# Kernel tuning notes

Hardware: AMD Instinct MI355X
Metric: run time of the kernel (lower is better)

## Reference

```python
import jax, jax.numpy as jnp
import numpy as np

ALPHA = 0.2   # LeakyReLU negative slope
NEG = -9e15   # mask fill value from the torch code


def _conv1d(x, w, b):
    # x: (N, C_in, L), w: (C_out, C_in, 5), padding=2 -> same length
    y = jax.lax.conv_general_dilated(x, w, window_strides=(1,), padding=[(2, 2)],
                                     dimension_numbers=('NCH', 'OIH', 'NCH'))
    return y + b[None, :, None]


def _gat(h, mask, W, a):
    # Faithful to a_input @ a: e_ij = leakyrelu(Wh_i . a[:H] + Wh_j . a[H:])
    Wh = jnp.einsum('bnf,fo->bno', h, W)          # (B,N,H)
    H = W.shape[1]
    f1 = Wh @ a[:H]                               # (B,N,1)
    f2 = Wh @ a[H:]                               # (B,N,1)
    e = f1 + jnp.swapaxes(f2, 1, 2)               # (B,N,N)
    e = jnp.where(e > 0, e, ALPHA * e)            # LeakyReLU
    e = jnp.where(mask, e, NEG)
    att = jax.nn.softmax(e, axis=-1)              # dropout skipped (eval mode)
    return jnp.einsum('bij,bjo->bio', att, Wh)


def setup_inputs() -> dict:
    key = jax.random.key(0)
    ks = jax.random.split(key, 14)
    B, S, N, H, E = 8, 200, 512, 64, 2048
    sc = 0.1
    return {
        'x': jax.random.normal(ks[0], (B, S, N * 2), dtype=jnp.float32),
        'adj': jax.random.randint(ks[1], (N, N), 0, 2, dtype=jnp.int32),
        'edge_index': jax.random.randint(ks[2], (E, 2), 0, N, dtype=jnp.int32),
        'conv1_w': jax.random.normal(ks[3], (H // 2, 2, 5), dtype=jnp.float32) * sc,
        'conv1_b': jnp.zeros((H // 2,), dtype=jnp.float32),
        'conv2_w': jax.random.normal(ks[4], (H, H // 2, 5), dtype=jnp.float32) * sc,
        'conv2_b': jnp.zeros((H,), dtype=jnp.float32),
        'W1': jax.random.normal(ks[5], (H, H), dtype=jnp.float32) * sc,
        'a1': jax.random.normal(ks[6], (2 * H, 1), dtype=jnp.float32) * sc,
        'W2': jax.random.normal(ks[7], (H, H), dtype=jnp.float32) * sc,
        'a2': jax.random.normal(ks[8], (2 * H, 1), dtype=jnp.float32) * sc,
        'fc1_w': jax.random.normal(ks[9], (2 * H, H), dtype=jnp.float32) * sc,
        'fc1_b': jnp.zeros((H,), dtype=jnp.float32),
        'fc2_w': jax.random.normal(ks[10], (H, 1), dtype=jnp.float32) * sc,
        'fc2_b': jnp.zeros((1,), dtype=jnp.float32),
    }


def reference(x, adj, edge_index, conv1_w, conv1_b, conv2_w, conv2_b,
              W1, a1, W2, a2, fc1_w, fc1_b, fc2_w, fc2_b):
    B = x.shape[0]
    N = adj.shape[0]
    # (B,S,2N) -> (B,N,S,2) -> (B*N,2,S)
    xn = x.reshape(B, -1, N, 2).transpose(0, 2, 1, 3)
    xf = xn.reshape(B * N, -1, 2).transpose(0, 2, 1)
    h = jax.nn.relu(_conv1d(xf, conv1_w, conv1_b))
    h = jax.nn.relu(_conv1d(h, conv2_w, conv2_b))
    h = h.mean(axis=-1)                 # AdaptiveAvgPool1d(1) + squeeze
    h = h.reshape(B, N, -1)             # (B,N,H)
    mask = (adj > 0)[None]              # (1,N,N) broadcasts over batch
    h = jax.nn.relu(_gat(h, mask, W1, a1))
    h = _gat(h, mask, W2, a2)
    h1 = h[:, edge_index[:, 0]]         # (B,E,H)
    h2 = h[:, edge_index[:, 1]]
    he = jnp.concatenate([h1, h2], axis=-1)  # (B,E,2H)
    z = jax.nn.relu(he @ fc1_w + fc1_b)
    return jax.nn.sigmoid(z @ fc2_w + fc2_b).squeeze(-1)  # (B,E)
```

## Files before the change

kernel.cpp:

```cpp
#include <hip/hip_runtime.h>
#include <hip/hip_bf16.h>

typedef unsigned short u16;
typedef __attribute__((ext_vector_type(8))) short short8;
typedef __attribute__((ext_vector_type(4))) float float4v;

#define BATCH 8
#define SLEN  200
#define NNODE 512
#define NEDGE 2048
#define NEGV  -9000000000000000.0f

#define H1S 40
#define H1R 212

__device__ __forceinline__ u16 f2bf(float f) {
    unsigned int x = __float_as_uint(f);
    unsigned int lsb = (x >> 16) & 1u;
    x += 0x7fffu + lsb;
    return (u16)(x >> 16);
}

__device__ __forceinline__ float bf2f(u16 u) {
    return __uint_as_float(((unsigned int)u) << 16);
}

__device__ __forceinline__ unsigned int pk2(float a, float b) {
    __hip_bfloat162 h = __float22bfloat162_rn(make_float2(a, b));
    unsigned int r;
    __builtin_memcpy(&r, &h, 4);
    return r;
}

__global__ __launch_bounds__(256) void pre_kernel(
    const float* __restrict__ x,
    const int* __restrict__ adj,
    const float* __restrict__ w2,
    const float* __restrict__ fc1w,
    const float* __restrict__ W2g,
    float* __restrict__ xT,
    u16* __restrict__ w2f,
    u16* __restrict__ efw,
    u16* __restrict__ w2gf,
    u16* __restrict__ msk)
{
    __shared__ float tile[32][33];
    const int t = threadIdx.x;
    const int blk = blockIdx.x;

    if (blk < 1792) {
        const int xi  = blk & 31;
        const int rem = blk >> 5;
        const int yi  = rem % 7;
        const int zi  = rem / 7;
        const int nc0 = xi * 32;
        const int s0  = yi * 32;
        const int c   = t & 31, rr = t >> 5;
        #pragma unroll
        for (int r = 0; r < 4; ++r) {
            const int s = s0 + rr + r * 8;
            if (s < SLEN)
                tile[rr + r * 8][c] = x[((size_t)(zi * SLEN + s)) * 1024 + nc0 + c];
        }
        __syncthreads();
        #pragma unroll
        for (int r = 0; r < 4; ++r) {
            const int nc = nc0 + rr + r * 8;
            const int s = s0 + c;
            if (s < SLEN)
                xT[((size_t)(zi * 1024 + nc)) * SLEN + s] = tile[c][rr + r * 8];
        }
        return;
    }

    if (blk == 1792) {
        for (int idx = t; idx < 20 * 64 * 8; idx += 256) {
            const int fid = idx >> 9, rem = idx & 511;
            const int lane = rem >> 3, j = rem & 7;
            const int kk = fid >> 2, ot = fid & 3;
            const int ml = lane & 15, q = lane >> 4;
            const int c  = q * 8 + j;
            const int ic = (c & 1) * 16 + (c >> 1);
            const int oc = ot * 16 + ml;
            w2f[idx] = f2bf(w2[(size_t)oc * 160 + ic * 5 + kk]);
        }
        return;
    }
    if (blk == 1793) {
        for (int idx = t; idx < 16 * 64 * 8; idx += 256) {
            const int u = idx >> 9, rem = idx & 511;
            const int lane = rem >> 3, j = rem & 7;
            const int ks = u >> 2, wvv = u & 3;
            const int ml = lane & 15, q = lane >> 4;
            const int o = wvv * 16 + ml;
            const int k = ks * 32 + q * 8 + j;
            efw[idx] = f2bf(fc1w[k * 64 + o]);
        }
        return;
    }
    if (blk == 1794) {
        for (int idx = t; idx < 8 * 64 * 8; idx += 256) {
            const int u = idx >> 9, rem = idx & 511;
            const int lane = rem >> 3, j = rem & 7;
            const int kh = u >> 2, nt = u & 3;
            const int ml = lane & 15, q = lane >> 4;
            const int o = nt * 16 + ml;
            const int k = kh * 32 + q * 8 + j;
            w2gf[idx] = f2bf(W2g[k * 64 + o]);
        }
        return;
    }

    {
        const int tid   = (blk - 1795) * 256 + t;
        const int row   = tid >> 5;
        const int chunk = tid & 31;
        const int4* ap = (const int4*)(adj + (size_t)row * 512 + chunk * 16);
        const int4 a0 = ap[0], a1 = ap[1], a2 = ap[2], a3 = ap[3];
        unsigned int bits = 0;
        bits |= (a0.x > 0) ? 0x0001u : 0u;  bits |= (a0.y > 0) ? 0x0002u : 0u;
        bits |= (a0.z > 0) ? 0x0004u : 0u;  bits |= (a0.w > 0) ? 0x0008u : 0u;
        bits |= (a1.x > 0) ? 0x0010u : 0u;  bits |= (a1.y > 0) ? 0x0020u : 0u;
        bits |= (a1.z > 0) ? 0x0040u : 0u;  bits |= (a1.w > 0) ? 0x0080u : 0u;
        bits |= (a2.x > 0) ? 0x0100u : 0u;  bits |= (a2.y > 0) ? 0x0200u : 0u;
        bits |= (a2.z > 0) ? 0x0400u : 0u;  bits |= (a2.w > 0) ? 0x0800u : 0u;
        bits |= (a3.x > 0) ? 0x1000u : 0u;  bits |= (a3.y > 0) ? 0x2000u : 0u;
        bits |= (a3.z > 0) ? 0x4000u : 0u;  bits |= (a3.w > 0) ? 0x8000u : 0u;
        msk[row * 32 + chunk] = (u16)bits;
    }
}

__global__ __launch_bounds__(256) void conv_fused_kernel(
    const float* __restrict__ xT,
    const float* __restrict__ w1,
    const float* __restrict__ b1,
    const float* __restrict__ b2,
    const float* __restrict__ W1,
    const float* __restrict__ a1,
    const u16* __restrict__ w2f,
    u16* __restrict__ Wh_bt,
    float* __restrict__ f1,
    float* __restrict__ f2)
{
    __shared__ float xs[2][2][212];
    __shared__ __align__(16) u16 h1p[H1R * H1S];
    __shared__ float red[4][2][32];
    __shared__ float hm[2][64];
    __shared__ float part[2][4][64];

    const int t    = threadIdx.x;
    const int blk  = blockIdx.x;
    const int b    = blk >> 8;
    const int pair = blk & 255;
    const int n0   = pair * 2;
    const int lane = t & 63;
    const int wv   = t >> 6;
    const int ml   = lane & 15;
    const int q    = lane >> 4;
    const int p = t & 15;
    const int g = t >> 4;
    const int o2 = wv & 1;
    const int mh = wv >> 1;

    short8 wfA[5], wfB[5];
    #pragma unroll
    for (int kk = 0; kk < 5; ++kk) {
        wfA[kk] = *(const short8*)(w2f + ((kk * 4 + o2 * 2 + 0) * 64 + lane) * 8);
        wfB[kk] = *(const short8*)(w2f + ((kk * 4 + o2 * 2 + 1) * 64 + lane) * 8);
    }
    const float bias2a = b2[o2 * 32 + ml];
    const float bias2b = b2[o2 * 32 + 16 + ml];

    float wA[10], wB[10];
    #pragma unroll
    for (int j = 0; j < 10; ++j) {
        wA[j] = w1[p * 10 + j];
        wB[j] = w1[(16 + p) * 10 + j];
    }
    const float b1a = b1[p], b1b = b1[16 + p];

    if (t < SLEN) {
        const float* xp = xT + ((size_t)(b * 1024 + 4 * pair)) * SLEN + t;
        xs[0][0][2 + t] = xp[0];
        xs[0][1][2 + t] = xp[SLEN];
        xs[1][0][2 + t] = xp[2 * SLEN];
        xs[1][1][2 + t] = xp[3 * SLEN];
    } else if (t < 212) {
        const int pp = (t < 202) ? (t - 200) : t;
        xs[0][0][pp] = 0.f; xs[0][1][pp] = 0.f;
        xs[1][0][pp] = 0.f; xs[1][1][pp] = 0.f;
    }
    {
        unsigned int* hz = (unsigned int*)h1p;
        if (t < 40)       hz[t] = 0u;
        else if (t < 240) hz[4000 + t] = 0u;
    }
    __syncthreads();

    float tAn[2], tBn[2];
    for (int nd = 0; nd < 2; ++nd) {
        #pragma unroll
        for (int u = 0; u < 4; ++u) {
            const int base = 4 * g + 64 * u;
            if (base < SLEN) {
                float X0[8], X1[8];
                *(float4*)&X0[0] = *(const float4*)&xs[nd][0][base];
                *(float4*)&X0[4] = *(const float4*)&xs[nd][0][base + 4];
                *(float4*)&X1[0] = *(const float4*)&xs[nd][1][base];
                *(float4*)&X1[4] = *(const float4*)&xs[nd][1][base + 4];
                #pragma unroll
                for (int i = 0; i < 4; ++i) {
                    float a0 = b1a, a1v = b1b;
                    #pragma unroll
                    for (int k = 0; k < 5; ++k) {
                        const float x0 = X0[i + k], x1 = X1[i + k];
                        a0  += wA[k] * x0 + wA[5 + k] * x1;
                        a1v += wB[k] * x0 + wB[5 + k] * x1;
                    }
                    *(unsigned int*)&h1p[(2 + base + i) * H1S + 2 * p] =
                        pk2(fmaxf(a0, 0.f), fmaxf(a1v, 0.f));
                }
            }
        }
        __syncthreads();

        float tA = 0.f, tB = 0.f;
        const int mt0 = mh * 7, mtE = mh ? 13 : 7;
        for (int mt = mt0; mt < mtE; ++mt) {
            float4v acc0 = {0.f, 0.f, 0.f, 0.f};
            float4v acc1 = {0.f, 0.f, 0.f, 0.f};
            #pragma unroll
            for (int kk = 0; kk < 5; ++kk) {
                const short8 a = *(const short8*)&h1p[(mt * 16 + ml + kk) * H1S + q * 8];
                acc0 = __builtin_amdgcn_mfma_f32_16x16x32_bf16(a, wfA[kk], acc0, 0, 0, 0);
                acc1 = __builtin_amdgcn_mfma_f32_16x16x32_bf16(a, wfB[kk], acc1, 0, 0, 0);
            }
            if (mt < 12) {
                #pragma unroll
                for (int r = 0; r < 4; ++r) {
                    tA += fmaxf(acc0[r] + bias2a, 0.f);
                    tB += fmaxf(acc1[r] + bias2b, 0.f);
                }
            } else if (q < 2) {
                #pragma unroll
                for (int r = 0; r < 4; ++r) {
                    tA += fmaxf(acc0[r] + bias2a, 0.f);
                    tB += fmaxf(acc1[r] + bias2b, 0.f);
                }
            }
        }
        tA += __shfl_xor(tA, 16, 64);
        tA += __shfl_xor(tA, 32, 64);
        tB += __shfl_xor(tB, 16, 64);
        tB += __shfl_xor(tB, 32, 64);
        tAn[nd] = tA;
        tBn[nd] = tB;
        __syncthreads();
    }

    if (lane < 16) {
        red[wv][0][ml]      = tAn[0];
        red[wv][0][16 + ml] = tBn[0];
        red[wv][1][ml]      = tAn[1];
        red[wv][1][16 + ml] = tBn[1];
    }
    __syncthreads();
    if (t < 128) {
        const int nd = t >> 6, o = t & 63;
        const int grp = (o >> 5), idx = o & 31;
        hm[nd][o] = (red[grp][nd][idx] + red[grp + 2][nd][idx]) * (1.0f / 200.0f);
    }
    __syncthreads();

    {
        const int o = t & 63, q4 = t >> 6;
        const float* Wp = W1 + (q4 * 16) * 64 + o;
        float p0 = 0.f, p1 = 0.f;
        #pragma unroll
        for (int k = 0; k < 16; ++k) {
            const float w = Wp[k * 64];
            p0 += hm[0][q4 * 16 + k] * w;
            p1 += hm[1][q4 * 16 + k] * w;
        }
        part[0][q4][o] = p0;
        part[1][q4][o] = p1;
    }
    __syncthreads();
    if (t < 128) {
        const int nd = t >> 6, o = t & 63;
        const int n = n0 + nd;
        const float v = part[nd][0][o] + part[nd][1][o] + part[nd][2][o] + part[nd][3][o];
        Wh_bt[((size_t)(b * 64 + o)) * 512 + n] = f2bf(v);
        float v1 = v * a1[o];
        float v2 = v * a1[64 + o];
        #pragma unroll
        for (int off = 32; off; off >>= 1) {
            v1 += __shfl_xor(v1, off, 64);
            v2 += __shfl_xor(v2, off, 64);
        }
        if (o == 0) { f1[b * 512 + n] = v1; f2[b * 512 + n] = v2; }
    }
}

#define PSTR 520
__global__ __launch_bounds__(512) void gat_attn_kernel(
    const u16* __restrict__ Wh_bt,
    const float* __restrict__ f1in,
    const float* __restrict__ f2in,
    const u16* __restrict__ msk,
    const u16* __restrict__ w2gf,
    const float* __restrict__ a2,
    u16* __restrict__ whbt_out,
    float* __restrict__ f1out,
    float* __restrict__ f2out,
    float* __restrict__ outp,
    const int fuse)
{
    __shared__ __align__(16) u16 P[16 * PSTR];
    __shared__ float f2s[512];
    __shared__ float invs[16];
    __shared__ float f1s[16];
    __shared__ float accH[4][64][4];
    __shared__ __align__(16) u16 g1s[16 * 72];
    __shared__ __align__(16) u16 wh2s[64 * 20];
    __shared__ float fp1[4][16], fp2[4][16];

    const int t   = threadIdx.x;
    const int blk = blockIdx.x;
    const int b   = blk >> 5;
    const int i0  = (blk & 31) * 16;
    const int lane = t & 63, wv = t >> 6, nt = wv & 3, kh = wv >> 2;
    const int ml = lane & 15, q = lane >> 4;

    const u16* Bp = Wh_bt + ((size_t)(b * 64 + nt * 16 + ml)) * 512 + kh * 256 + q * 8;
    short8 bfr[8];
    #pragma unroll
    for (int ks = 0; ks < 8; ++ks)
        bfr[ks] = *(const short8*)(Bp + ks * 32);

    f2s[t & 511] = f2in[b * 512 + (t & 511)];
    if (t < 16) f1s[t] = f1in[b * 512 + i0 + t];
    __syncthreads();

    {
        const int i = t >> 5, jseg = t & 31;
        const float f1i = f1s[i];
        const unsigned int mbits = msk[(size_t)(i0 + i) * 32 + jseg];
        const float* f2p = f2s + jseg * 16;
        float ev[16];
        float mx = -3.0e38f;
        #pragma unroll
        for (int v = 0; v < 16; ++v) {
            float e = f1i + f2p[v];
            e = e > 0.f ? e : 0.2f * e;
            e = ((mbits >> v) & 1u) ? e : NEGV;
            ev[v] = e;
            mx = fmaxf(mx, e);
        }
        mx = fmaxf(mx, __shfl_xor(mx, 1, 64));
        mx = fmaxf(mx, __shfl_xor(mx, 2, 64));
        mx = fmaxf(mx, __shfl_xor(mx, 4, 64));
        mx = fmaxf(mx, __shfl_xor(mx, 8, 64));
        mx = fmaxf(mx, __shfl_xor(mx, 16, 64));
        float sum = 0.f;
        #pragma unroll
        for (int v = 0; v < 16; ++v) {
            const float ex = __expf(ev[v] - mx);
            ev[v] = ex;
            sum += ex;
        }
        sum += __shfl_xor(sum, 1, 64);
        sum += __shfl_xor(sum, 2, 64);
        sum += __shfl_xor(sum, 4, 64);
        sum += __shfl_xor(sum, 8, 64);
        sum += __shfl_xor(sum, 16, 64);
        if (jseg == 0) invs[i] = 1.0f / sum;
        unsigned int* prow = (unsigned int*)&P[i * PSTR + jseg * 16];
        #pragma unroll
        for (int v = 0; v < 8; ++v)
            prow[v] = pk2(ev[2 * v], ev[2 * v + 1]);
    }
    __syncthreads();

    float4v acc = {0.f, 0.f, 0.f, 0.f};
    #pragma unroll
    for (int ks = 0; ks < 8; ++ks) {
        const short8 afr = *(const short8*)&P[ml * PSTR + kh * 256 + ks * 32 + q * 8];
        acc = __builtin_amdgcn_mfma_f32_16x16x32_bf16(afr, bfr[ks], acc, 0, 0, 0);
    }
    if (kh == 1) {
        #pragma unroll
        for (int r = 0; r < 4; ++r) accH[nt][lane][r] = acc[r];
    }
    __syncthreads();
    if (kh == 0) {
        #pragma unroll
        for (int r = 0; r < 4; ++r) {
            const int i2 = q * 4 + r;
            float val = (acc[r] + accH[nt][lane][r]) * invs[i2];
            if (fuse) {
                val = fmaxf(val, 0.f);
                g1s[i2 * 72 + nt * 16 + ml] = f2bf(val);
            } else {
                outp[((size_t)(b * 512 + i0 + i2)) * 64 + nt * 16 + ml] = val;
            }
        }
    }

    if (!fuse) return;

    __syncthreads();
    const short8 af2 = *(const short8*)&g1s[ml * 72 + kh * 32 + q * 8];
    const short8 bf2v = *(const short8*)(w2gf + ((kh * 4 + nt) * 64 + lane) * 8);
    float4v c2 = {0.f, 0.f, 0.f, 0.f};
    c2 = __builtin_amdgcn_mfma_f32_16x16x32_bf16(af2, bf2v, c2, 0, 0, 0);
    if (kh == 1) {
        #pragma unroll
        for (int r = 0; r < 4; ++r) accH[nt][lane][r] = c2[r];
    }
    __syncthreads();
    if (kh == 0) {
        const int o = nt * 16 + ml;
        const float a2o1 = a2[o], a2o2 = a2[64 + o];
        #pragma unroll
        for (int r = 0; r < 4; ++r) {
            const float wv2 = c2[r] + accH[nt][lane][r];
            wh2s[o * 20 + q * 4 + r] = f2bf(wv2);
            float p1 = wv2 * a2o1, p2 = wv2 * a2o2;
            p1 += __shfl_xor(p1, 1, 64); p2 += __shfl_xor(p2, 1, 64);
            p1 += __shfl_xor(p1, 2, 64); p2 += __shfl_xor(p2, 2, 64);
            p1 += __shfl_xor(p1, 4, 64); p2 += __shfl_xor(p2, 4, 64);
            p1 += __shfl_xor(p1, 8, 64); p2 += __shfl_xor(p2, 8, 64);
            if (ml == 0) {
                fp1[nt][q * 4 + r] = p1;
                fp2[nt][q * 4 + r] = p2;
            }
        }
    }
    __syncthreads();
    if (t < 256) {
        const int o = t >> 2, seg = t & 3;
        *(uint2*)&whbt_out[((size_t)(b * 64 + o)) * 512 + i0 + seg * 4] =
            *(const uint2*)&wh2s[o * 20 + seg * 4];
    }
    if (t < 16) {
        f1out[b * 512 + i0 + t] = fp1[0][t] + fp1[1][t] + fp1[2][t] + fp1[3][t];
        f2out[b * 512 + i0 + t] = fp2[0][t] + fp2[1][t] + fp2[2][t] + fp2[3][t];
    }
}

#define FSTR 136
__global__ __launch_bounds__(256) void edge_mlp_kernel(
    const float* __restrict__ hg,
    const int* __restrict__ eidx,
    const u16* __restrict__ efw,
    const float* __restrict__ fc1b,
    const float* __restrict__ fc2w,
    const float* __restrict__ fc2b,
    float* __restrict__ out)
{
    __shared__ __align__(16) u16 he[16 * FSTR];
    __shared__ float part[16][4];

    const int t   = threadIdx.x;
    const int blk = blockIdx.x;
    const int b   = blk >> 7;
    const int e0  = (blk & 127) * 16;
    const int lane = t & 63, wv = t >> 6, ml = lane & 15, q = lane >> 4;

    short8 bw[4];
    #pragma unroll
    for (int ks = 0; ks < 4; ++ks)
        bw[ks] = *(const short8*)(efw + ((ks * 4 + wv) * 64 + lane) * 8);
    const int o = 16 * wv + ml;
    const float bo = fc1b[o];
    const float wo = fc2w[o];

    {
        const int ep = t >> 4, p = t & 15;
        const int e = e0 + ep;
        const int node = (p < 8) ? eidx[e * 2] : eidx[e * 2 + 1];
        const int c0 = (p & 7) * 8;
        const float* hp = hg + ((size_t)(b * 512 + node)) * 64 + c0;
        const float4 fa = *(const float4*)hp;
        const float4 fb = *(const float4*)(hp + 4);
        unsigned int* dst = (unsigned int*)&he[ep * FSTR + ((p < 8) ? 0 : 64) + c0];
        dst[0] = pk2(fa.x, fa.y);
        dst[1] = pk2(fa.z, fa.w);
        dst[2] = pk2(fb.x, fb.y);
        dst[3] = pk2(fb.z, fb.w);
    }
    __syncthreads();

    float4v acc = {0.f, 0.f, 0.f, 0.f};
    #pragma unroll
    for (int ks = 0; ks < 4; ++ks) {
        const short8 afr = *(const short8*)&he[ml * FSTR + ks * 32 + q * 8];
        acc = __builtin_amdgcn_mfma_f32_16x16x32_bf16(afr, bw[ks], acc, 0, 0, 0);
    }
    #pragma unroll
    for (int r = 0; r < 4; ++r) {
        float z = fmaxf(acc[r] + bo, 0.f) * wo;
        z += __shfl_xor(z, 1, 64);
        z += __shfl_xor(z, 2, 64);
        z += __shfl_xor(z, 4, 64);
        z += __shfl_xor(z, 8, 64);
        if (ml == 0) part[q * 4 + r][wv] = z;
    }
    __syncthreads();
    if (t < 16) {
        const float v = part[t][0] + part[t][1] + part[t][2] + part[t][3] + fc2b[0];
        out[b * 2048 + e0 + t] = 1.0f / (1.0f + __expf(-v));
    }
}

extern "C" void kernel_launch(void* const* d_in, const int* in_sizes, int n_in,
                              void* d_out, int out_size, void* d_ws, size_t ws_size,
                              hipStream_t stream) {
    const float* x    = (const float*)d_in[0];
    const int* adj    = (const int*)d_in[1];
    const int* eidx   = (const int*)d_in[2];
    const float* w1   = (const float*)d_in[3];
    const float* b1   = (const float*)d_in[4];
    const float* w2   = (const float*)d_in[5];
    const float* b2   = (const float*)d_in[6];
    const float* W1   = (const float*)d_in[7];
    const float* a1   = (const float*)d_in[8];
    const float* W2   = (const float*)d_in[9];
    const float* a2   = (const float*)d_in[10];
    const float* fc1w = (const float*)d_in[11];
    const float* fc1b = (const float*)d_in[12];
    const float* fc2w = (const float*)d_in[13];
    const float* fc2b = (const float*)d_in[14];
    float* out = (float*)d_out;

    float* ws = (float*)d_ws;
    const size_t R = (size_t)BATCH * NNODE;
    float* g     = ws;
    float* f1a   = g + R * 64;
    float* f2a   = f1a + R;
    float* f1b   = f2a + R;
    float* f2b   = f1b + R;
    u16*   whbt1 = (u16*)(f2b + R);
    u16*   whbt2 = whbt1 + R * 64;
    u16*   w2f   = whbt2 + R * 64;
    u16*   efw   = w2f + 10240;
    u16*   w2gf  = efw + 8192;
    u16*   msk   = w2gf + 4096;
    float* xT    = (float*)(msk + 16384);

    pre_kernel<<<dim3(1859), dim3(256), 0, stream>>>(
        x, adj, w2, fc1w, W2, xT, w2f, efw, w2gf, msk);
    conv_fused_kernel<<<dim3(2048), dim3(256), 0, stream>>>(
        xT, w1, b1, b2, W1, a1, w2f, whbt1, f1a, f2a);
    gat_attn_kernel<<<dim3(256), dim3(512), 0, stream>>>(
        whbt1, f1a, f2a, msk, w2gf, a2, whbt2, f1b, f2b, g, 1);
    gat_attn_kernel<<<dim3(256), dim3(512), 0, stream>>>(
        whbt2, f1b, f2b, msk, w2gf, a2, whbt2, f1b, f2b, g, 0);
    edge_mlp_kernel<<<dim3(1024), dim3(256), 0, stream>>>(
        g, eidx, efw, fc1b, fc2w, fc2b, out);
}
```

Before: 136.6 us.

## Drop x transpose pass and fuse both GAT layers with edge MLP cooperatively

The separate transpose of x into xT is removed. The conv kernel now reads four contiguous floats per timestep directly from x with a float4 load. The two GAT attention launches and the edge MLP launch are merged into one cooperative kernel that uses grid-wide syncs between layers, and each block handles 64 edges in the MLP stage. This removes a full-size transpose write/read and two kernel launches. In exchange, x reads become strided in the conv kernel, and the merged kernel pays for grid syncs and a larger shared-memory footprint.

Result: slower. 279.8 us (+104.9%).

```diff
diff --git a/kernel.cpp b/kernel.cpp
--- a/kernel.cpp
+++ b/kernel.cpp
@@ -1,5 +1,8 @@
 #include <hip/hip_runtime.h>
 #include <hip/hip_bf16.h>
+#include <hip/hip_cooperative_groups.h>
+
+namespace cg = cooperative_groups;
 
 typedef unsigned short u16;
 typedef __attribute__((ext_vector_type(8))) short short8;
@@ -33,47 +36,19 @@
 }
 
 __global__ __launch_bounds__(256) void pre_kernel(
-    const float* __restrict__ x,
     const int* __restrict__ adj,
     const float* __restrict__ w2,
     const float* __restrict__ fc1w,
     const float* __restrict__ W2g,
-    float* __restrict__ xT,
     u16* __restrict__ w2f,
     u16* __restrict__ efw,
     u16* __restrict__ w2gf,
     u16* __restrict__ msk)
 {
-    __shared__ float tile[32][33];
     const int t = threadIdx.x;
     const int blk = blockIdx.x;
 
-    if (blk < 1792) {
-        const int xi  = blk & 31;
-        const int rem = blk >> 5;
-        const int yi  = rem % 7;
-        const int zi  = rem / 7;
-        const int nc0 = xi * 32;
-        const int s0  = yi * 32;
-        const int c   = t & 31, rr = t >> 5;
-        #pragma unroll
-        for (int r = 0; r < 4; ++r) {
-            const int s = s0 + rr + r * 8;
-            if (s < SLEN)
-                tile[rr + r * 8][c] = x[((size_t)(zi * SLEN + s)) * 1024 + nc0 + c];
-        }
-        __syncthreads();
-        #pragma unroll
-        for (int r = 0; r < 4; ++r) {
-            const int nc = nc0 + rr + r * 8;
-            const int s = s0 + c;
-            if (s < SLEN)
-                xT[((size_t)(zi * 1024 + nc)) * SLEN + s] = tile[c][rr + r * 8];
-        }
-        return;
-    }
-
-    if (blk == 1792) {
+    if (blk == 0) {
         for (int idx = t; idx < 20 * 64 * 8; idx += 256) {
             const int fid = idx >> 9, rem = idx & 511;
             const int lane = rem >> 3, j = rem & 7;
@@ -86,7 +61,7 @@
         }
         return;
     }
-    if (blk == 1793) {
+    if (blk == 1) {
         for (int idx = t; idx < 16 * 64 * 8; idx += 256) {
             const int u = idx >> 9, rem = idx & 511;
             const int lane = rem >> 3, j = rem & 7;
@@ -98,7 +73,7 @@
         }
         return;
     }
-    if (blk == 1794) {
+    if (blk == 2) {
         for (int idx = t; idx < 8 * 64 * 8; idx += 256) {
             const int u = idx >> 9, rem = idx & 511;
             const int lane = rem >> 3, j = rem & 7;
@@ -112,7 +87,7 @@
     }
 
     {
-        const int tid   = (blk - 1795) * 256 + t;
+        const int tid   = (blk - 3) * 256 + t;
         const int row   = tid >> 5;
         const int chunk = tid & 31;
         const int4* ap = (const int4*)(adj + (size_t)row * 512 + chunk * 16);
@@ -131,7 +106,7 @@
 }
 
 __global__ __launch_bounds__(256) void conv_fused_kernel(
-    const float* __restrict__ xT,
+    const float* __restrict__ x,
     const float* __restrict__ w1,
     const float* __restrict__ b1,
     const float* __restrict__ b2,
@@ -180,11 +155,11 @@
     const float b1a = b1[p], b1b = b1[16 + p];
 
     if (t < SLEN) {
-        const float* xp = xT + ((size_t)(b * 1024 + 4 * pair)) * SLEN + t;
-        xs[0][0][2 + t] = xp[0];
-        xs[0][1][2 + t] = xp[SLEN];
-        xs[1][0][2 + t] = xp[2 * SLEN];
-        xs[1][1][2 + t] = xp[3 * SLEN];
+        const float4 xv = *(const float4*)(x + ((size_t)(b * SLEN + t)) * 1024 + 4 * pair);
+        xs[0][0][2 + t] = xv.x;
+        xs[0][1][2 + t] = xv.y;
+        xs[1][0][2 + t] = xv.z;
+        xs[1][1][2 + t] = xv.w;
     } else if (t < 212) {
         const int pp = (t < 202) ? (t - 200) : t;
         xs[0][0][pp] = 0.f; xs[0][1][pp] = 0.f;
@@ -303,19 +278,27 @@
 }
 
 #define PSTR 520
-__global__ __launch_bounds__(512) void gat_attn_kernel(
-    const u16* __restrict__ Wh_bt,
-    const float* __restrict__ f1in,
-    const float* __restrict__ f2in,
+#define FSTR 136
+__global__ __launch_bounds__(512) void gat_edge_kernel(
+    const u16* __restrict__ Wh1,
+    const float* __restrict__ f1a,
+    const float* __restrict__ f2a,
     const u16* __restrict__ msk,
     const u16* __restrict__ w2gf,
     const float* __restrict__ a2,
-    u16* __restrict__ whbt_out,
-    float* __restrict__ f1out,
-    float* __restrict__ f2out,
-    float* __restrict__ outp,
-    const int fuse)
+    u16* __restrict__ Wh2,
+    float* __restrict__ f1b,
+    float* __restrict__ f2b,
+    float* __restrict__ g,
+    const int* __restrict__ eidx,
+    const u16* __restrict__ efw,
+    const float* __restrict__ fc1b,
+    const float* __restrict__ fc2w,
+    const float* __restrict__ fc2b,
+    float* __restrict__ out)
 {
+    cg::grid_group gg = cg::this_grid();
+
     __shared__ __align__(16) u16 P[16 * PSTR];
     __shared__ float f2s[512];
     __shared__ float invs[16];
@@ -324,6 +307,8 @@
     __shared__ __align__(16) u16 g1s[16 * 72];
     __shared__ __align__(16) u16 wh2s[64 * 20];
     __shared__ float fp1[4][16], fp2[4][16];
+    __shared__ __align__(16) u16 he[64 * FSTR];
+    __shared__ float epart[4][16][4];
 
     const int t   = threadIdx.x;
     const int blk = blockIdx.x;
@@ -332,159 +317,150 @@
     const int lane = t & 63, wv = t >> 6, nt = wv & 3, kh = wv >> 2;
     const int ml = lane & 15, q = lane >> 4;
 
-    const u16* Bp = Wh_bt + ((size_t)(b * 64 + nt * 16 + ml)) * 512 + kh * 256 + q * 8;
-    short8 bfr[8];
-    #pragma unroll
-    for (int ks = 0; ks < 8; ++ks)
-        bfr[ks] = *(const short8*)(Bp + ks * 32);
-
-    f2s[t & 511] = f2in[b * 512 + (t & 511)];
-    if (t < 16) f1s[t] = f1in[b * 512 + i0 + t];
-    __syncthreads();
-
-    {
-        const int i = t >> 5, jseg = t & 31;
-        const float f1i = f1s[i];
-        const unsigned int mbits = msk[(size_t)(i0 + i) * 32 + jseg];
-        const float* f2p = f2s + jseg * 16;
-        float ev[16];
-        float mx = -3.0e38f;
-        #pragma unroll
-        for (int v = 0; v < 16; ++v) {
-            float e = f1i + f2p[v];
-            e = e > 0.f ? e : 0.2f * e;
-            e = ((mbits >> v) & 1u) ? e : NEGV;
-            ev[v] = e;
-            mx = fmaxf(mx, e);
-        }
-        mx = fmaxf(mx, __shfl_xor(mx, 1, 64));
-        mx = fmaxf(mx, __shfl_xor(mx, 2, 64));
-        mx = fmaxf(mx, __shfl_xor(mx, 4, 64));
-        mx = fmaxf(mx, __shfl_xor(mx, 8, 64));
-        mx = fmaxf(mx, __shfl_xor(mx, 16, 64));
-        float sum = 0.f;
-        #pragma unroll
-        for (int v = 0; v < 16; ++v) {
-            const float ex = __expf(ev[v] - mx);
-            ev[v] = ex;
-            sum += ex;
-        }
-        sum += __shfl_xor(sum, 1, 64);
-        sum += __shfl_xor(sum, 2, 64);
-        sum += __shfl_xor(sum, 4, 64);
-        sum += __shfl_xor(sum, 8, 64);
-        sum += __shfl_xor(sum, 16, 64);
-        if (jseg == 0) invs[i] = 1.0f / sum;
-        unsigned int* prow = (unsigned int*)&P[i * PSTR + jseg * 16];
-        #pragma unroll
-        for (int v = 0; v < 8; ++v)
-            prow[v] = pk2(ev[2 * v], ev[2 * v + 1]);
-    }
-    __syncthreads();
-
-    float4v acc = {0.f, 0.f, 0.f, 0.f};
-    #pragma unroll
-    for (int ks = 0; ks < 8; ++ks) {
-        const short8 afr = *(const short8*)&P[ml * PSTR + kh * 256 + ks * 32 + q * 8];
-        acc = __builtin_amdgcn_mfma_f32_16x16x32_bf16(afr, bfr[ks], acc, 0, 0, 0);
-    }
-    if (kh == 1) {
-        #pragma unroll
-        for (int r = 0; r < 4; ++r) accH[nt][lane][r] = acc[r];
-    }
-    __syncthreads();
-    if (kh == 0) {
-        #pragma unroll
-        for (int r = 0; r < 4; ++r) {
-            const int i2 = q * 4 + r;
-            float val = (acc[r] + accH[nt][lane][r]) * invs[i2];
-            if (fuse) {
-                val = fmaxf(val, 0.f);
-                g1s[i2 * 72 + nt * 16 + ml] = f2bf(val);
-            } else {
-                outp[((size_t)(b * 512 + i0 + i2)) * 64 + nt * 16 + ml] = val;
-            }
-        }
-    }
-
-    if (!fuse) return;
-
-    __syncthreads();
-    const short8 af2 = *(const short8*)&g1s[ml * 72 + kh * 32 + q * 8];
-    const short8 bf2v = *(const short8*)(w2gf + ((kh * 4 + nt) * 64 + lane) * 8);
-    float4v c2 = {0.f, 0.f, 0.f, 0.f};
-    c2 = __builtin_amdgcn_mfma_f32_16x16x32_bf16(af2, bf2v, c2, 0, 0, 0);
-    if (kh == 1) {
-        #pragma unroll
-        for (int r = 0; r < 4; ++r) accH[nt][lane][r] = c2[r];
-    }
-    __syncthreads();
-    if (kh == 0) {
-        const int o = nt * 16 + ml;
-        const float a2o1 = a2[o], a2o2 = a2[64 + o];
-        #pragma unroll
-        for (int r = 0; r < 4; ++r) {
-            const float wv2 = c2[r] + accH[nt][lane][r];
-            wh2s[o * 20 + q * 4 + r] = f2bf(wv2);
-            float p1 = wv2 * a2o1, p2 = wv2 * a2o2;
-            p1 += __shfl_xor(p1, 1, 64); p2 += __shfl_xor(p2, 1, 64);
-            p1 += __shfl_xor(p1, 2, 64); p2 += __shfl_xor(p2, 2, 64);
-            p1 += __shfl_xor(p1, 4, 64); p2 += __shfl_xor(p2, 4, 64);
-            p1 += __shfl_xor(p1, 8, 64); p2 += __shfl_xor(p2, 8, 64);
-            if (ml == 0) {
-                fp1[nt][q * 4 + r] = p1;
-                fp2[nt][q * 4 + r] = p2;
-            }
-        }
-    }
-    __syncthreads();
-    if (t < 256) {
-        const int o = t >> 2, seg = t & 3;
-        *(uint2*)&whbt_out[((size_t)(b * 64 + o)) * 512 + i0 + seg * 4] =
-            *(const uint2*)&wh2s[o * 20 + seg * 4];
-    }
-    if (t < 16) {
-        f1out[b * 512 + i0 + t] = fp1[0][t] + fp1[1][t] + fp1[2][t] + fp1[3][t];
-        f2out[b * 512 + i0 + t] = fp2[0][t] + fp2[1][t] + fp2[2][t] + fp2[3][t];
-    }
-}
-
-#define FSTR 136
-__global__ __launch_bounds__(256) void edge_mlp_kernel(
-    const float* __restrict__ hg,
-    const int* __restrict__ eidx,
-    const u16* __restrict__ efw,
-    const float* __restrict__ fc1b,
-    const float* __restrict__ fc2w,
-    const float* __restrict__ fc2b,
-    float* __restrict__ out)
-{
-    __shared__ __align__(16) u16 he[16 * FSTR];
-    __shared__ float part[16][4];
-
-    const int t   = threadIdx.x;
-    const int blk = blockIdx.x;
-    const int b   = blk >> 7;
-    const int e0  = (blk & 127) * 16;
-    const int lane = t & 63, wv = t >> 6, ml = lane & 15, q = lane >> 4;
+    for (int layer = 0; layer < 2; ++layer) {
+        const u16*   WhIn = layer ? Wh2 : Wh1;
+        const float* f1in = layer ? f1b : f1a;
+        const float* f2in = layer ? f2b : f2a;
+
+        const u16* Bp = WhIn + ((size_t)(b * 64 + nt * 16 + ml)) * 512 + kh * 256 + q * 8;
+        short8 bfr[8];
+        #pragma unroll
+        for (int ks = 0; ks < 8; ++ks)
+            bfr[ks] = *(const short8*)(Bp + ks * 32);
+
+        f2s[t & 511] = f2in[b * 512 + (t & 511)];
+        if (t < 16) f1s[t] = f1in[b * 512 + i0 + t];
+        __syncthreads();
+
+        {
+            const int i = t >> 5, jseg = t & 31;
+            const float f1i = f1s[i];
+            const unsigned int mbits = msk[(size_t)(i0 + i) * 32 + jseg];
+            const float* f2p = f2s + jseg * 16;
+            float ev[16];
+            float mx = -3.0e38f;
+            #pragma unroll
+            for (int v = 0; v < 16; ++v) {
+                float e = f1i + f2p[v];
+                e = e > 0.f ? e : 0.2f * e;
+                e = ((mbits >> v) & 1u) ? e : NEGV;
+                ev[v] = e;
+                mx = fmaxf(mx, e);
+            }
+            mx = fmaxf(mx, __shfl_xor(mx, 1, 64));
+            mx = fmaxf(mx, __shfl_xor(mx, 2, 64));
+            mx = fmaxf(mx, __shfl_xor(mx, 4, 64));
+            mx = fmaxf(mx, __shfl_xor(mx, 8, 64));
+            mx = fmaxf(mx, __shfl_xor(mx, 16, 64));
+            float sum = 0.f;
+            #pragma unroll
+            for (int v = 0; v < 16; ++v) {
+                const float ex = __expf(ev[v] - mx);
+                ev[v] = ex;
+                sum += ex;
+            }
+            sum += __shfl_xor(sum, 1, 64);
+            sum += __shfl_xor(sum, 2, 64);
+            sum += __shfl_xor(sum, 4, 64);
+            sum += __shfl_xor(sum, 8, 64);
+            sum += __shfl_xor(sum, 16, 64);
+            if (jseg == 0) invs[i] = 1.0f / sum;
+            unsigned int* prow = (unsigned int*)&P[i * PSTR + jseg * 16];
+            #pragma unroll
+            for (int v = 0; v < 8; ++v)
+                prow[v] = pk2(ev[2 * v], ev[2 * v + 1]);
+        }
+        __syncthreads();
+
+        float4v acc = {0.f, 0.f, 0.f, 0.f};
+        #pragma unroll
+        for (int ks = 0; ks < 8; ++ks) {
+            const short8 afr = *(const short8*)&P[ml * PSTR + kh * 256 + ks * 32 + q * 8];
+            acc = __builtin_amdgcn_mfma_f32_16x16x32_bf16(afr, bfr[ks], acc, 0, 0, 0);
+        }
+        if (kh == 1) {
+            #pragma unroll
+            for (int r = 0; r < 4; ++r) accH[nt][lane][r] = acc[r];
+        }
+        __syncthreads();
+        if (kh == 0) {
+            #pragma unroll
+            for (int r = 0; r < 4; ++r) {
+                const int i2 = q * 4 + r;
+                float val = (acc[r] + accH[nt][lane][r]) * invs[i2];
+                if (layer == 0) {
+                    val = fmaxf(val, 0.f);
+                    g1s[i2 * 72 + nt * 16 + ml] = f2bf(val);
+                } else {
+                    g[((size_t)(b * 512 + i0 + i2)) * 64 + nt * 16 + ml] = val;
+                }
+            }
+        }
+
+        if (layer == 0) {
+            __syncthreads();
+            const short8 af2 = *(const short8*)&g1s[ml * 72 + kh * 32 + q * 8];
+            const short8 bf2v = *(const short8*)(w2gf + ((kh * 4 + nt) * 64 + lane) * 8);
+            float4v c2 = {0.f, 0.f, 0.f, 0.f};
+            c2 = __builtin_amdgcn_mfma_f32_16x16x32_bf16(af2, bf2v, c2, 0, 0, 0);
+            if (kh == 1) {
+                #pragma unroll
+                for (int r = 0; r < 4; ++r) accH[nt][lane][r] = c2[r];
+            }
+            __syncthreads();
+            if (kh == 0) {
+                const int o = nt * 16 + ml;
+                const float a2o1 = a2[o], a2o2 = a2[64 + o];
+                #pragma unroll
+                for (int r = 0; r < 4; ++r) {
+                    const float wv2 = c2[r] + accH[nt][lane][r];
+                    wh2s[o * 20 + q * 4 + r] = f2bf(wv2);
+                    float p1 = wv2 * a2o1, p2 = wv2 * a2o2;
+                    p1 += __shfl_xor(p1, 1, 64); p2 += __shfl_xor(p2, 1, 64);
+                    p1 += __shfl_xor(p1, 2, 64); p2 += __shfl_xor(p2, 2, 64);
+                    p1 += __shfl_xor(p1, 4, 64); p2 += __shfl_xor(p2, 4, 64);
+                    p1 += __shfl_xor(p1, 8, 64); p2 += __shfl_xor(p2, 8, 64);
+                    if (ml == 0) {
+                        fp1[nt][q * 4 + r] = p1;
+                        fp2[nt][q * 4 + r] = p2;
+                    }
+                }
+            }
+            __syncthreads();
+            if (t < 256) {
+                const int o = t >> 2, seg = t & 3;
+                *(uint2*)&Wh2[((size_t)(b * 64 + o)) * 512 + i0 + seg * 4] =
+                    *(const uint2*)&wh2s[o * 20 + seg * 4];
+            }
+            if (t < 16) {
+                f1b[b * 512 + i0 + t] = fp1[0][t] + fp1[1][t] + fp1[2][t] + fp1[3][t];
+                f2b[b * 512 + i0 + t] = fp2[0][t] + fp2[1][t] + fp2[2][t] + fp2[3][t];
+            }
+        }
+        __threadfence();
+        gg.sync();
+    }
 
     short8 bw[4];
     #pragma unroll
     for (int ks = 0; ks < 4; ++ks)
-        bw[ks] = *(const short8*)(efw + ((ks * 4 + wv) * 64 + lane) * 8);
-    const int o = 16 * wv + ml;
+        bw[ks] = *(const short8*)(efw + ((ks * 4 + nt) * 64 + lane) * 8);
+    const int o = nt * 16 + ml;
     const float bo = fc1b[o];
     const float wo = fc2w[o];
 
-    {
-        const int ep = t >> 4, p = t & 15;
-        const int e = e0 + ep;
-        const int node = (p < 8) ? eidx[e * 2] : eidx[e * 2 + 1];
-        const int c0 = (p & 7) * 8;
-        const float* hp = hg + ((size_t)(b * 512 + node)) * 64 + c0;
+    #pragma unroll
+    for (int it = 0; it < 2; ++it) {
+        const int idx = it * 512 + t;
+        const int ep = idx >> 4, pp = idx & 15;
+        const int gidx = blk * 64 + ep;
+        const int bb = gidx >> 11, ee = gidx & 2047;
+        const int node = (pp < 8) ? eidx[ee * 2] : eidx[ee * 2 + 1];
+        const int c0 = (pp & 7) * 8;
+        const float* hp = g + ((size_t)(bb * 512 + node)) * 64 + c0;
         const float4 fa = *(const float4*)hp;
         const float4 fb = *(const float4*)(hp + 4);
-        unsigned int* dst = (unsigned int*)&he[ep * FSTR + ((p < 8) ? 0 : 64) + c0];
+        unsigned int* dst = (unsigned int*)&he[ep * FSTR + ((pp < 8) ? 0 : 64) + c0];
         dst[0] = pk2(fa.x, fa.y);
         dst[1] = pk2(fa.z, fa.w);
         dst[2] = pk2(fb.x, fb.y);
@@ -492,25 +468,29 @@
     }
     __syncthreads();
 
-    float4v acc = {0.f, 0.f, 0.f, 0.f};
-    #pragma unroll
-    for (int ks = 0; ks < 4; ++ks) {
-        const short8 afr = *(const short8*)&he[ml * FSTR + ks * 32 + q * 8];
-        acc = __builtin_amdgcn_mfma_f32_16x16x32_bf16(afr, bw[ks], acc, 0, 0, 0);
-    }
-    #pragma unroll
-    for (int r = 0; r < 4; ++r) {
-        float z = fmaxf(acc[r] + bo, 0.f) * wo;
-        z += __shfl_xor(z, 1, 64);
-        z += __shfl_xor(z, 2, 64);
-        z += __shfl_xor(z, 4, 64);
-        z += __shfl_xor(z, 8, 64);
-        if (ml == 0) part[q * 4 + r][wv] = z;
+    for (int grp = kh; grp < 4; grp += 2) {
+        float4v acc = {0.f, 0.f, 0.f, 0.f};
+        #pragma unroll
+        for (int ks = 0; ks < 4; ++ks) {
+            const short8 afr = *(const short8*)&he[(grp * 16 + ml) * FSTR + ks * 32 + q * 8];
+            acc = __builtin_amdgcn_mfma_f32_16x16x32_bf16(afr, bw[ks], acc, 0, 0, 0);
+        }
+        #pragma unroll
+        for (int r = 0; r < 4; ++r) {
+            float z = fmaxf(acc[r] + bo, 0.f) * wo;
+            z += __shfl_xor(z, 1, 64);
+            z += __shfl_xor(z, 2, 64);
+            z += __shfl_xor(z, 4, 64);
+            z += __shfl_xor(z, 8, 64);
+            if (ml == 0) epart[grp][q * 4 + r][nt] = z;
+        }
     }
     __syncthreads();
-    if (t < 16) {
-        const float v = part[t][0] + part[t][1] + part[t][2] + part[t][3] + fc2b[0];
-        out[b * 2048 + e0 + t] = 1.0f / (1.0f + __expf(-v));
+    if (t < 64) {
+        const int grp = t >> 4, el = t & 15;
+        const float v = epart[grp][el][0] + epart[grp][el][1]
+                      + epart[grp][el][2] + epart[grp][el][3] + fc2b[0];
+        out[blk * 64 + grp * 16 + el] = 1.0f / (1.0f + __expf(-v));
     }
 }
 
@@ -547,16 +527,35 @@
     u16*   efw   = w2f + 10240;
     u16*   w2gf  = efw + 8192;
     u16*   msk   = w2gf + 4096;
-    float* xT    = (float*)(msk + 16384);
-
-    pre_kernel<<<dim3(1859), dim3(256), 0, stream>>>(
-        x, adj, w2, fc1w, W2, xT, w2f, efw, w2gf, msk);
+
+    pre_kernel<<<dim3(67), dim3(256), 0, stream>>>(
+        adj, w2, fc1w, W2, w2f, efw, w2gf, msk);
     conv_fused_kernel<<<dim3(2048), dim3(256), 0, stream>>>(
-        xT, w1, b1, b2, W1, a1, w2f, whbt1, f1a, f2a);
-    gat_attn_kernel<<<dim3(256), dim3(512), 0, stream>>>(
-        whbt1, f1a, f2a, msk, w2gf, a2, whbt2, f1b, f2b, g, 1);
-    gat_attn_kernel<<<dim3(256), dim3(512), 0, stream>>>(
-        whbt2, f1b, f2b, msk, w2gf, a2, whbt2, f1b, f2b, g, 0);
-    edge_mlp_kernel<<<dim3(1024), dim3(256), 0, stream>>>(
-        g, eidx, efw, fc1b, fc2w, fc2b, out);
-}
+        x, w1, b1, b2, W1, a1, w2f, whbt1, f1a, f2a);
+    {
+        const u16*   a_whbt1 = whbt1;
+        const float* a_f1a = f1a;
+        const float* a_f2a = f2a;
+        const u16*   a_msk = msk;
+        const u16*   a_w2gf = w2gf;
+        const float* a_a2 = a2;
+        u16*   a_whbt2 = whbt2;
+        float* a_f1b = f1b;
+        float* a_f2b = f2b;
+        float* a_g = g;
+        const int* a_eidx = eidx;
+        const u16* a_efw = efw;
+        const float* a_fc1b = fc1b;
+        const float* a_fc2w = fc2w;
+        const float* a_fc2b = fc2b;
+        float* a_out = out;
+        void* args[] = {
+            (void*)&a_whbt1, (void*)&a_f1a, (void*)&a_f2a, (void*)&a_msk,
+            (void*)&a_w2gf, (void*)&a_a2, (void*)&a_whbt2, (void*)&a_f1b,
+            (void*)&a_f2b, (void*)&a_g, (void*)&a_eidx, (void*)&a_efw,
+            (void*)&a_fc1b, (void*)&a_fc2w, (void*)&a_fc2b, (void*)&a_out
+        };
+        hipLaunchCooperativeKernel((void*)gat_edge_kernel, dim3(256), dim3(512),
+                                   args, 0, stream);
+    }
+}
```
